# Optimization experiments

Measured on AMD Instinct MI355X. Metric: run time of the kernel, lower is better.

## Reference

```python
import jax, jax.numpy as jnp
import numpy as np
from jax import lax

B, C, H, W = 8, 256, 128, 128
RED = 4  # SE reduction


def setup_inputs() -> dict:
    key = jax.random.key(0)
    ks = jax.random.split(key, 7)
    s = 0.05
    return {
        "x": jax.random.normal(ks[0], (B, C, H, W), dtype=jnp.float32),
        "w_deform": jax.random.normal(ks[1], (C, C, 3, 3), dtype=jnp.float32) * s,
        "b_deform": jax.random.normal(ks[2], (C,), dtype=jnp.float32) * s,
        "w_se1": jax.random.normal(ks[3], (C // RED, C), dtype=jnp.float32) * s,
        "b_se1": jax.random.normal(ks[4], (C // RED,), dtype=jnp.float32) * s,
        "w_se2": jax.random.normal(ks[5], (C, C // RED), dtype=jnp.float32) * s,
        "b_se2": jax.random.normal(ks[6], (C,), dtype=jnp.float32) * s,
    }


def reference(x, w_deform, b_deform, w_se1, b_se1, w_se2, b_se2):
    # DeformConv2d with the all-zero offset tensor used in forward(): bilinear
    # sampling at integer taps == standard 3x3 conv, padding=1, zero-padded borders.
    y = lax.conv_general_dilated(
        x, w_deform,
        window_strides=(1, 1),
        padding=((1, 1), (1, 1)),
        dimension_numbers=("NCHW", "OIHW", "NCHW"),
    ) + b_deform[None, :, None, None]  # [B, C, H, W]

    # SE: global average pool -> 1x1 conv -> ReLU -> 1x1 conv -> sigmoid
    p = y.mean(axis=(2, 3))                                   # [B, C]
    h = jax.nn.relu(p @ w_se1.T + b_se1)                      # [B, C//RED]
    scale = jax.nn.sigmoid(h @ w_se2.T + b_se2)               # [B, C]
    return y * scale[:, :, None, None]
```

## Files before the change

kernel.cpp:

```cpp
#include <hip/hip_runtime.h>
#include <hip/hip_bf16.h>

#define BB 8
#define CC 256
#define HH 128
#define WW 128

typedef __attribute__((ext_vector_type(8))) short bf16x8;
typedef __attribute__((ext_vector_type(4))) float f32x4;

static __device__ __forceinline__ unsigned short f2bf(float f) {
  unsigned int u = __builtin_bit_cast(unsigned int, f);
  u += 0x7fffu + ((u >> 16) & 1u);
  return (unsigned short)(u >> 16);
}

static __device__ __forceinline__ void async16(const void* g, void* l) {
#if __has_builtin(__builtin_amdgcn_global_load_lds)
  __builtin_amdgcn_global_load_lds(
      (__attribute__((address_space(1))) void*)(unsigned long long)(g),
      (__attribute__((address_space(3))) void*)(unsigned int)(unsigned long long)(l),
      16, 0, 0);
#else
  *(bf16x8*)l = *(const bf16x8*)g;
#endif
}

__global__ __launch_bounds__(256) void k_convert_w(const float* __restrict__ w,
                                                   unsigned short* __restrict__ Wt,
                                                   float* __restrict__ sums) {
  __shared__ unsigned short lw[8 * 2304];
  const int t = threadIdx.x;
  const int co0 = blockIdx.x << 3;
  for (int z = blockIdx.x * 256 + t; z < 18432; z += 8192) sums[z] = 0.f;
  const float* src = w + co0 * 2304;
  for (int k = t; k < 18432; k += 256) lw[k] = f2bf(src[k]);
  __syncthreads();
  for (int g = t; g < 18432; g += 256) {
    const int tap = g >> 11, rem = g & 2047;
    const int o = rem >> 6, rem2 = rem & 63;
    const int cl = rem2 >> 3, e = rem2 & 7;
    Wt[(((tap << 5) + o) << 11) + ((co0 + cl) << 3) + e] =
        lw[cl * 2304 + ((o << 3) + e) * 9 + tap];
  }
}

__global__ __launch_bounds__(256) void k_transpose_x(const float* __restrict__ x,
                                                     unsigned short* __restrict__ Xc,
                                                     float* __restrict__ sums) {
  __shared__ float tile[64][65];
  const int t = threadIdx.x;
  const int bz = blockIdx.z;
  const int b = bz >> 7, h = bz & 127;
  const int c0 = blockIdx.y << 6, w0 = blockIdx.x << 6;
  const float* xp = x + (((b * CC) * HH) + h) * WW;
#pragma unroll
  for (int i = 0; i < 4; ++i) {
    int idx = t + (i << 8);
    int cr = idx >> 4, wq = idx & 15;
    float4 v = *(const float4*)(xp + (c0 + cr) * (HH * WW) + w0 + (wq << 2));
    tile[cr][(wq << 2) + 0] = v.x;
    tile[cr][(wq << 2) + 1] = v.y;
    tile[cr][(wq << 2) + 2] = v.z;
    tile[cr][(wq << 2) + 3] = v.w;
  }
  __syncthreads();
  const int ob = c0 >> 3;
#pragma unroll
  for (int i = 0; i < 2; ++i) {
    int g = t + (i << 8);
    int o = g >> 6, wr = g & 63;
    bf16x8 v;
#pragma unroll
    for (int e = 0; e < 8; ++e) v[e] = (short)f2bf(tile[(o << 3) + e][wr]);
    *(bf16x8*)(Xc + ((((b << 7) + h) * 32) + ob + o) * 1024 + (w0 + wr) * 8) = v;
  }
  {
    const int c = t >> 2, seg = t & 3;
    float s = 0.f;
#pragma unroll
    for (int k = 0; k < 16; ++k) s += tile[c][(seg << 4) + k];
    s += __shfl_xor(s, 1);
    s += __shfl_xor(s, 2);
    const int ci = b * CC + c0 + c;
    if (seg == 0) {
      atomicAdd(&sums[ci], s);
      if (h == 0)   atomicAdd(&sums[2048 + ci], s);
      if (h == 127) atomicAdd(&sums[4096 + ci], s);
      if (w0 == 0) {
        atomicAdd(&sums[6144 + ci], tile[c][0]);
        if (h == 0)   atomicAdd(&sums[10240 + ci], tile[c][0]);
        if (h == 127) atomicAdd(&sums[14336 + ci], tile[c][0]);
      }
    }
    if (seg == 3 && w0 == 64) {
      atomicAdd(&sums[8192 + ci], tile[c][63]);
      if (h == 0)   atomicAdd(&sums[12288 + ci], tile[c][63]);
      if (h == 127) atomicAdd(&sums[16384 + ci], tile[c][63]);
    }
  }
}

__global__ __launch_bounds__(256) void k_pool2(const float* __restrict__ w,
                                               const float* __restrict__ bd,
                                               const float* __restrict__ sums,
                                               float* __restrict__ p_buf) {
  __shared__ float ts[2304];
  const int b = blockIdx.y, t = threadIdx.x;
  const int lane = t & 63, wid = t >> 6;
  {
    const int ci = (b << 8) + t;
    const float S  = sums[ci];
    const float R0 = sums[2048 + ci], R1 = sums[4096 + ci];
    const float C0 = sums[6144 + ci], C1 = sums[8192 + ci];
    const float x00 = sums[10240 + ci], x0W = sums[12288 + ci];
    const float xH0 = sums[14336 + ci], xHW = sums[16384 + ci];
    const float er[3] = {R1, 0.f, R0};
    const float ec[3] = {C1, 0.f, C0};
    const float cor[9] = {xHW, 0.f, xH0, 0.f, 0.f, 0.f, x0W, 0.f, x00};
#pragma unroll
    for (int kh = 0; kh < 3; ++kh)
#pragma unroll
      for (int kw = 0; kw < 3; ++kw)
        ts[t * 9 + kh * 3 + kw] = S - er[kh] - ec[kw] + cor[kh * 3 + kw];
  }
  __syncthreads();
  float4 tv[9];
#pragma unroll
  for (int q = 0; q < 9; ++q) tv[q] = *(const float4*)&ts[(q * 64 + lane) * 4];
  const int co = (blockIdx.x << 3) + (wid << 1);
#pragma unroll
  for (int c2 = 0; c2 < 2; ++c2) {
    const float4* wr = (const float4*)(w + (co + c2) * 2304) + lane;
    float s = 0.f;
#pragma unroll
    for (int q = 0; q < 9; ++q) {
      float4 wv = wr[q * 64];
      s += wv.x * tv[q].x + wv.y * tv[q].y + wv.z * tv[q].z + wv.w * tv[q].w;
    }
    s += __shfl_xor(s, 1);  s += __shfl_xor(s, 2);  s += __shfl_xor(s, 4);
    s += __shfl_xor(s, 8);  s += __shfl_xor(s, 16); s += __shfl_xor(s, 32);
    if (lane == 0) p_buf[(b << 8) + co + c2] = bd[co + c2] + s * (1.0f / 16384.0f);
  }
}

__global__ __launch_bounds__(256) void k_se2(const float* __restrict__ p_buf,
                                             const float* __restrict__ w1,
                                             const float* __restrict__ b1,
                                             const float* __restrict__ w2,
                                             const float* __restrict__ b2,
                                             float* __restrict__ scale) {
  __shared__ float p[CC];
  __shared__ float h1[64];
  const int b = blockIdx.x, t = threadIdx.x;
  const int lane = t & 63, wid = t >> 6;
  p[t] = p_buf[(b << 8) + t];
  __syncthreads();
  {
    const float4 pv = *(const float4*)&p[lane << 2];
#pragma unroll
    for (int i = 0; i < 16; ++i) {
      const int r = (wid << 4) + i;
      float4 wv = ((const float4*)(w1 + (r << 8)))[lane];
      float s = wv.x * pv.x + wv.y * pv.y + wv.z * pv.z + wv.w * pv.w;
      s += __shfl_xor(s, 1);  s += __shfl_xor(s, 2);  s += __shfl_xor(s, 4);
      s += __shfl_xor(s, 8);  s += __shfl_xor(s, 16); s += __shfl_xor(s, 32);
      if (lane == 0) {
        float v = b1[r] + s;
        h1[r] = v > 0.f ? v : 0.f;
      }
    }
  }
  __syncthreads();
  {
    float s = b2[t];
    const float* wr = w2 + (t << 6);
#pragma unroll
    for (int k = 0; k < 64; ++k) s += wr[k] * h1[k];
    scale[(b << 8) + t] = 1.0f / (1.0f + expf(-s));
  }
}

__global__ __launch_bounds__(256, 3) void k_conv(
    const unsigned short* __restrict__ Xc, const unsigned short* __restrict__ Wt,
    const float* __restrict__ bias, const float* __restrict__ scale,
    float* __restrict__ out) {
  __shared__ __align__(16) unsigned short Xs[2 * 12480];
  const int t = threadIdx.x;
  const int lin = (blockIdx.y << 1) | blockIdx.x;
  const int Wk = ((lin & 7) << 8) | (lin >> 3);
  const int m0 = (Wk & 1) << 7;
  const int bh = Wk >> 1;
  const int b = bh >> 7, h = bh & 127;
  const int lane = t & 63, wid = t >> 6;
  const int wave_m = (wid & 1) << 6, wave_n = (wid >> 1) << 6;
  const int n0 = lane & 15, quad = lane >> 4;
  const int part = wid & 1, rsel = wid >> 1;

  bf16x8 z8 = {0, 0, 0, 0, 0, 0, 0, 0};
  if (t < 48) {
    int bi = t / 24, rem = t % 24;
    int dh = rem >> 3, rem2 = rem & 7, q = rem2 >> 1, side = rem2 & 1;
    *(bf16x8*)&Xs[bi * 12480 + dh * 4160 + q * 1040 + (side ? 1032 : 0)] = z8;
  }
  if (h == 0 || h == 127) {
    const int dhz = (h == 0) ? 0 : 2;
    for (int g = t; g < 1040; g += 256) {
      int bi = g >= 520, gg = g - bi * 520;
      *(bf16x8*)&Xs[bi * 12480 + dhz * 4160 + gg * 8] = z8;
    }
  }

  auto stage = [&](int cb8, int bi) {
    const int ob = cb8 << 2;
#pragma unroll
    for (int r = 0; r < 6; ++r) {
      const int rr = (r << 1) | rsel;
      const int dh = rr >> 2, q = rr & 3;
      const int hh = h - 1 + dh;
      if (hh >= 0 && hh < HH) {
        const unsigned short* gp =
            Xc + ((((b << 7) + hh) * 32 + ob + q) << 10) + (part << 9) + (lane << 3);
        unsigned short* lp =
            &Xs[bi * 12480 + dh * 4160 + q * 1040 + 8 + (part << 9) + (lane << 3)];
        async16(gp, lp);
      }
    }
  };

  f32x4 acc[4][4];
  f32x4 zero4 = {0.f, 0.f, 0.f, 0.f};
#pragma unroll
  for (int i = 0; i < 4; ++i)
#pragma unroll
    for (int j = 0; j < 4; ++j) acc[i][j] = zero4;

  stage(0, 0);
  __syncthreads();

  for (int cb8 = 0; cb8 < 8; ++cb8) {
    const int cur = cb8 & 1;
    if (cb8 < 7) stage(cb8 + 1, cur ^ 1);
    const unsigned short* wb =
        Wt + ((((cb8 << 2) + quad) << 8) + m0 + wave_m + n0) * 8;
    const unsigned short* xb = &Xs[cur * 12480 + quad * 1040 + (wave_n + n0) * 8];

    bf16x8 af[3][4], bg[2][4];
#pragma unroll
    for (int i = 0; i < 4; ++i) af[0][i] = *(const bf16x8*)(wb + i * 128);
#pragma unroll
    for (int i = 0; i < 4; ++i) af[1][i] = *(const bf16x8*)(wb + 65536 + i * 128);
#pragma unroll
    for (int j = 0; j < 4; ++j) bg[0][j] = *(const bf16x8*)(xb + (j << 4) * 8);

#pragma unroll
    for (int tap = 0; tap < 9; ++tap) {
      if (tap < 7) {
#pragma unroll
        for (int i = 0; i < 4; ++i)
          af[(tap + 2) % 3][i] = *(const bf16x8*)(wb + (tap + 2) * 65536 + i * 128);
      }
      if (tap < 8) {
        const int kh1 = (tap + 1) / 3, kw1 = (tap + 1) % 3;
#pragma unroll
        for (int j = 0; j < 4; ++j)
          bg[(tap + 1) & 1][j] =
              *(const bf16x8*)(xb + kh1 * 4160 + ((j << 4) + kw1) * 8);
      }
#pragma unroll
      for (int i = 0; i < 4; ++i)
#pragma unroll
        for (int j = 0; j < 4; ++j)
          acc[i][j] = __builtin_amdgcn_mfma_f32_16x16x32_bf16(
              af[tap % 3][i], bg[tap & 1][j], acc[i][j], 0, 0, 0);
    }
    __syncthreads();
  }

#pragma unroll
  for (int i = 0; i < 4; ++i) {
    const int mrow = m0 + wave_m + (i << 4) + (quad << 2);
    float bs[4], ss[4];
#pragma unroll
    for (int r = 0; r < 4; ++r) {
      bs[r] = bias[mrow + r];
      ss[r] = scale[(b << 8) + mrow + r];
    }
#pragma unroll
    for (int j = 0; j < 4; ++j) {
      const int wcol = wave_n + (j << 4) + n0;
      float* op = out + ((((b << 8) + mrow) * HH) + h) * WW + wcol;
#pragma unroll
      for (int r = 0; r < 4; ++r)
        op[r * (HH * WW)] = (acc[i][j][r] + bs[r]) * ss[r];
    }
  }
}

extern "C" void kernel_launch(void* const* d_in, const int* in_sizes, int n_in,
                              void* d_out, int out_size, void* d_ws, size_t ws_size,
                              hipStream_t stream) {
  const float* x  = (const float*)d_in[0];
  const float* wd = (const float*)d_in[1];
  const float* bd = (const float*)d_in[2];
  const float* w1 = (const float*)d_in[3];
  const float* b1 = (const float*)d_in[4];
  const float* w2 = (const float*)d_in[5];
  const float* b2 = (const float*)d_in[6];
  float* out = (float*)d_out;

  char* ws = (char*)d_ws;
  unsigned short* Xc = (unsigned short*)ws;
  unsigned short* Wt = (unsigned short*)(ws + 67108864);
  float* sums  = (float*)(ws + 68288512);
  float* p_buf = (float*)(ws + 68362240);
  float* scale = (float*)(ws + 68370432);

  k_convert_w<<<dim3(32), dim3(256), 0, stream>>>(wd, Wt, sums);
  k_transpose_x<<<dim3(2, 4, 1024), dim3(256), 0, stream>>>(x, Xc, sums);
  k_pool2<<<dim3(32, 8), dim3(256), 0, stream>>>(wd, bd, sums, p_buf);
  k_se2<<<dim3(8), dim3(256), 0, stream>>>(p_buf, w1, b1, w2, b2, scale);
  k_conv<<<dim3(2, 1024), dim3(256), 0, stream>>>(Xc, Wt, bd, scale, out);
}
```

Baseline: 413.4 us.

## Compute two output rows per conv block to reuse weight fragments

```diff
diff --git a/kernel.cpp b/kernel.cpp
--- a/kernel.cpp
+++ b/kernel.cpp
@@ -181,59 +181,62 @@
   }
 }
 
-__global__ __launch_bounds__(256, 3) void k_conv(
+__global__ __launch_bounds__(256, 2) void k_conv(
     const unsigned short* __restrict__ Xc, const unsigned short* __restrict__ Wt,
     const float* __restrict__ bias, const float* __restrict__ scale,
     float* __restrict__ out) {
-  __shared__ __align__(16) unsigned short Xs[2 * 12480];
+  extern __shared__ __align__(16) unsigned short Xs[];
   const int t = threadIdx.x;
   const int lin = (blockIdx.y << 1) | blockIdx.x;
-  const int Wk = ((lin & 7) << 8) | (lin >> 3);
+  const int Wk = ((lin & 7) << 7) | (lin >> 3);
   const int m0 = (Wk & 1) << 7;
-  const int bh = Wk >> 1;
-  const int b = bh >> 7, h = bh & 127;
+  const int bhp = Wk >> 1;
+  const int b = bhp >> 6;
+  const int h0 = (bhp & 63) << 1;
   const int lane = t & 63, wid = t >> 6;
   const int wave_m = (wid & 1) << 6, wave_n = (wid >> 1) << 6;
   const int n0 = lane & 15, quad = lane >> 4;
   const int part = wid & 1, rsel = wid >> 1;
 
   bf16x8 z8 = {0, 0, 0, 0, 0, 0, 0, 0};
-  if (t < 48) {
-    int bi = t / 24, rem = t % 24;
+  if (t < 64) {
+    int bi = t >> 5, rem = t & 31;
     int dh = rem >> 3, rem2 = rem & 7, q = rem2 >> 1, side = rem2 & 1;
-    *(bf16x8*)&Xs[bi * 12480 + dh * 4160 + q * 1040 + (side ? 1032 : 0)] = z8;
-  }
-  if (h == 0 || h == 127) {
-    const int dhz = (h == 0) ? 0 : 2;
+    *(bf16x8*)&Xs[bi * 16640 + dh * 4160 + q * 1040 + (side ? 1032 : 0)] = z8;
+  }
+  if (h0 == 0 || h0 == 126) {
+    const int dhz = (h0 == 0) ? 0 : 3;
     for (int g = t; g < 1040; g += 256) {
       int bi = g >= 520, gg = g - bi * 520;
-      *(bf16x8*)&Xs[bi * 12480 + dhz * 4160 + gg * 8] = z8;
+      *(bf16x8*)&Xs[bi * 16640 + dhz * 4160 + gg * 8] = z8;
     }
   }
 
   auto stage = [&](int cb8, int bi) {
     const int ob = cb8 << 2;
 #pragma unroll
-    for (int r = 0; r < 6; ++r) {
+    for (int r = 0; r < 8; ++r) {
       const int rr = (r << 1) | rsel;
       const int dh = rr >> 2, q = rr & 3;
-      const int hh = h - 1 + dh;
+      const int hh = h0 - 1 + dh;
       if (hh >= 0 && hh < HH) {
         const unsigned short* gp =
             Xc + ((((b << 7) + hh) * 32 + ob + q) << 10) + (part << 9) + (lane << 3);
         unsigned short* lp =
-            &Xs[bi * 12480 + dh * 4160 + q * 1040 + 8 + (part << 9) + (lane << 3)];
+            &Xs[bi * 16640 + dh * 4160 + q * 1040 + 8 + (part << 9) + (lane << 3)];
         async16(gp, lp);
       }
     }
   };
 
-  f32x4 acc[4][4];
+  f32x4 acc[2][4][4];
   f32x4 zero4 = {0.f, 0.f, 0.f, 0.f};
 #pragma unroll
-  for (int i = 0; i < 4; ++i)
-#pragma unroll
-    for (int j = 0; j < 4; ++j) acc[i][j] = zero4;
+  for (int r = 0; r < 2; ++r)
+#pragma unroll
+    for (int i = 0; i < 4; ++i)
+#pragma unroll
+      for (int j = 0; j < 4; ++j) acc[r][i][j] = zero4;
 
   stage(0, 0);
   __syncthreads();
@@ -243,36 +246,41 @@
     if (cb8 < 7) stage(cb8 + 1, cur ^ 1);
     const unsigned short* wb =
         Wt + ((((cb8 << 2) + quad) << 8) + m0 + wave_m + n0) * 8;
-    const unsigned short* xb = &Xs[cur * 12480 + quad * 1040 + (wave_n + n0) * 8];
-
-    bf16x8 af[3][4], bg[2][4];
+    const unsigned short* xb = &Xs[cur * 16640 + quad * 1040 + (wave_n + n0) * 8];
+
+    bf16x8 af[2][4], bg[2][4];
 #pragma unroll
     for (int i = 0; i < 4; ++i) af[0][i] = *(const bf16x8*)(wb + i * 128);
 #pragma unroll
-    for (int i = 0; i < 4; ++i) af[1][i] = *(const bf16x8*)(wb + 65536 + i * 128);
-#pragma unroll
     for (int j = 0; j < 4; ++j) bg[0][j] = *(const bf16x8*)(xb + (j << 4) * 8);
 
 #pragma unroll
-    for (int tap = 0; tap < 9; ++tap) {
-      if (tap < 7) {
+    for (int t9 = 0; t9 < 9; ++t9) {
+#pragma unroll
+      for (int r2 = 0; r2 < 2; ++r2) {
+        const int s = t9 * 2 + r2;
+        if (s < 17) {
+          const int sn = s + 1;
+          const int rn = sn & 1, tn = sn >> 1;
+          const int khn = tn / 3, kwn = tn % 3;
+#pragma unroll
+          for (int j = 0; j < 4; ++j)
+            bg[sn & 1][j] =
+                *(const bf16x8*)(xb + (rn + khn) * 4160 + ((j << 4) + kwn) * 8);
+        }
+        if (r2 == 0 && t9 < 8) {
+#pragma unroll
+          for (int i = 0; i < 4; ++i)
+            af[(t9 + 1) & 1][i] =
+                *(const bf16x8*)(wb + (t9 + 1) * 65536 + i * 128);
+        }
 #pragma unroll
         for (int i = 0; i < 4; ++i)
-          af[(tap + 2) % 3][i] = *(const bf16x8*)(wb + (tap + 2) * 65536 + i * 128);
-      }
-      if (tap < 8) {
-        const int kh1 = (tap + 1) / 3, kw1 = (tap + 1) % 3;
-#pragma unroll
-        for (int j = 0; j < 4; ++j)
-          bg[(tap + 1) & 1][j] =
-              *(const bf16x8*)(xb + kh1 * 4160 + ((j << 4) + kw1) * 8);
-      }
-#pragma unroll
-      for (int i = 0; i < 4; ++i)
-#pragma unroll
-        for (int j = 0; j < 4; ++j)
-          acc[i][j] = __builtin_amdgcn_mfma_f32_16x16x32_bf16(
-              af[tap % 3][i], bg[tap & 1][j], acc[i][j], 0, 0, 0);
+#pragma unroll
+          for (int j = 0; j < 4; ++j)
+            acc[r2][i][j] = __builtin_amdgcn_mfma_f32_16x16x32_bf16(
+                af[t9 & 1][i], bg[s & 1][j], acc[r2][i][j], 0, 0, 0);
+      }
     }
     __syncthreads();
   }
@@ -282,18 +290,20 @@
     const int mrow = m0 + wave_m + (i << 4) + (quad << 2);
     float bs[4], ss[4];
 #pragma unroll
-    for (int r = 0; r < 4; ++r) {
-      bs[r] = bias[mrow + r];
-      ss[r] = scale[(b << 8) + mrow + r];
-    }
-#pragma unroll
-    for (int j = 0; j < 4; ++j) {
-      const int wcol = wave_n + (j << 4) + n0;
-      float* op = out + ((((b << 8) + mrow) * HH) + h) * WW + wcol;
-#pragma unroll
-      for (int r = 0; r < 4; ++r)
-        op[r * (HH * WW)] = (acc[i][j][r] + bs[r]) * ss[r];
-    }
+    for (int r4 = 0; r4 < 4; ++r4) {
+      bs[r4] = bias[mrow + r4];
+      ss[r4] = scale[(b << 8) + mrow + r4];
+    }
+#pragma unroll
+    for (int r = 0; r < 2; ++r)
+#pragma unroll
+      for (int j = 0; j < 4; ++j) {
+        const int wcol = wave_n + (j << 4) + n0;
+        float* op = out + ((((b << 8) + mrow) * HH) + h0 + r) * WW + wcol;
+#pragma unroll
+        for (int r4 = 0; r4 < 4; ++r4)
+          op[r4 * (HH * WW)] = (acc[r][i][j][r4] + bs[r4]) * ss[r4];
+      }
   }
 }
 
@@ -316,9 +326,12 @@
   float* p_buf = (float*)(ws + 68362240);
   float* scale = (float*)(ws + 68370432);
 
+  (void)hipFuncSetAttribute((const void*)k_conv,
+                            hipFuncAttributeMaxDynamicSharedMemorySize, 66560);
+
   k_convert_w<<<dim3(32), dim3(256), 0, stream>>>(wd, Wt, sums);
   k_transpose_x<<<dim3(2, 4, 1024), dim3(256), 0, stream>>>(x, Xc, sums);
   k_pool2<<<dim3(32, 8), dim3(256), 0, stream>>>(wd, bd, sums, p_buf);
   k_se2<<<dim3(8), dim3(256), 0, stream>>>(p_buf, w1, b1, w2, b2, scale);
-  k_conv<<<dim3(2, 1024), dim3(256), 0, stream>>>(Xc, Wt, bd, scale, out);
-}
+  k_conv<<<dim3(2, 512), dim3(256), 66560, stream>>>(Xc, Wt, bd, scale, out);
+}
```

New measurement: 389.4 us. 1.06x faster.
